# Kernel tuning notes

Hardware: AMD Instinct MI355X
Metric: run time of the kernel (lower is better)

## Reference

```python
import jax, jax.numpy as jnp
import numpy as np

NUM_ENTITIES = 100000
NUM_RELATIONS = 500
D = 256            # embedding_dim
T = 4              # num_hash_tables
H = 32             # hash_dim
B = 64             # batch of queries
K = 10
CAND = max(K * 10, int(NUM_ENTITIES * 0.1))  # = 10000


def setup_inputs() -> dict:
    key = jax.random.key(0)
    k0, k1, k2, k3, k4 = jax.random.split(key, 5)
    return {
        "head": jax.random.randint(k0, (B,), 0, NUM_ENTITIES),
        "relation": jax.random.randint(k1, (B,), 0, NUM_RELATIONS),
        "entity_emb": jax.random.normal(k2, (NUM_ENTITIES, D), jnp.float32) * 0.02,
        "relation_emb": jax.random.normal(k3, (NUM_RELATIONS, D), jnp.float32) * 0.02,
        "hash_proj": jax.random.normal(k4, (T, D, H), jnp.float32),
        "k": K,
    }


def reference(head, relation, entity_emb, relation_emb, hash_proj, k):
    # DistMult approximate query path of KnowledgeGraph.query (use_approximate=True).
    h = entity_emb[head]            # [B, D]
    r = relation_emb[relation]      # [B, D]
    target = h * r                  # DistMult target embedding [B, D]

    # LSH hash codes (0/1 floats): projected > 0
    thash = (jnp.einsum('bd,tdh->bth', target, hash_proj) > 0).astype(jnp.float32)      # [B,T,H]
    ahash = (jnp.einsum('nd,tdh->nth', entity_emb, hash_proj) > 0).astype(jnp.float32)  # [N,T,H]

    # Hamming distance over (T,H) bits without materializing [B,N,T,H]:
    # mismatches = sum(a) + sum(b) - 2 * <a,b>  for 0/1 codes
    dot = jnp.einsum('bth,nth->bn', thash, ahash)                                        # [B,N]
    hash_dist = thash.sum((1, 2))[:, None] + ahash.sum((1, 2))[None, :] - 2.0 * dot      # [B,N]

    # top num_candidates with SMALLEST hamming distance
    _, cand_idx = jax.lax.top_k(-hash_dist, CAND)                                        # [B,CAND]

    # DistMult score: (h*r*t).sum(-1) == target . t ; compute dense then gather candidates
    scores_all = jnp.einsum('bd,nd->bn', target, entity_emb)                             # [B,N]
    cand_scores = jnp.take_along_axis(scores_all, cand_idx, axis=1)                      # [B,CAND]

    top_scores, top_local = jax.lax.top_k(cand_scores, k)                                # [B,k]
    top_indices = jnp.take_along_axis(cand_idx, top_local, axis=1)                       # [B,k]
    return top_indices, top_scores
```

## Files before the change

kernel.cpp:

```cpp
#include <hip/hip_runtime.h>
#include <hip/hip_bf16.h>
#include <float.h>

constexpr int NENT  = 100000;
constexpr int DDIM  = 256;
constexpr int BQ    = 64;
constexpr int CANDN = 10000;
constexpr int KTOP  = 10;
constexpr int NSLICE = 16;
constexpr int SLICE  = 6272;
constexpr int HPAD   = 132;

typedef short v8s __attribute__((ext_vector_type(8)));
typedef float v4f __attribute__((ext_vector_type(4)));

__device__ inline void split3(float x, unsigned short& h0, unsigned short& h1,
                              unsigned short& h2) {
    unsigned t0 = __float_as_uint(x) & 0xffff0000u;
    float r1 = x - __uint_as_float(t0);
    unsigned t1 = __float_as_uint(r1) & 0xffff0000u;
    float r2 = r1 - __uint_as_float(t1);
    h0 = (unsigned short)(t0 >> 16);
    h1 = (unsigned short)(t1 >> 16);
    h2 = (unsigned short)(__float_as_uint(r2) >> 16);
}

__device__ inline void split8p(const float* p0, const float* p1,
                               v8s& o0, v8s& o1, v8s& o2) {
    union { v8s v; unsigned short u[8]; } r0, r1, r2;
    float4 f0 = *(const float4*)p0;
    float4 f1 = *(const float4*)(p1);
    float av[8] = {f0.x, f0.y, f0.z, f0.w, f1.x, f1.y, f1.z, f1.w};
    #pragma unroll
    for (int j = 0; j < 8; j++)
        split3(av[j], r0.u[j], r1.u[j], r2.u[j]);
    o0 = r0.v; o1 = r1.v; o2 = r2.v;
}

__device__ inline void stage16(const float* g, float* l) {
    __builtin_amdgcn_global_load_lds(
        (const __attribute__((address_space(1))) void*)g,
        (__attribute__((address_space(3))) void*)l, 16, 0, 0);
}

__global__ __launch_bounds__(256) void k_prep(
    const int* __restrict__ head, const int* __restrict__ rel,
    const float* __restrict__ E, const float* __restrict__ Rm,
    const float* __restrict__ proj,
    float* __restrict__ tgtT, unsigned* __restrict__ thash,
    unsigned short* __restrict__ Whi, unsigned short* __restrict__ Wmid,
    unsigned short* __restrict__ Wlo)
{
    __shared__ float tg[DDIM];
    int blk = blockIdx.x;
    int tid = threadIdx.x;
    if (blk < 128) {
        int c = blk, d = tid;
        float x = proj[((c >> 5)*DDIM + d)*32 + (c & 31)];
        unsigned short h0, h1, h2;
        split3(x, h0, h1, h2);
        Whi [c*DDIM + d] = h0;
        Wmid[c*DDIM + d] = h1;
        Wlo [c*DDIM + d] = h2;
    } else {
        int b = blk - 128;
        int h = head[b], r = rel[b];
        int d = tid;
        float v = E[h*DDIM + d] * Rm[r*DDIM + d];
        tg[d] = v;
        tgtT[d*BQ + b] = v;
        unsigned short h0, h1, h2;
        split3(v, h0, h1, h2);
        int c = 128 + b;
        Whi [c*DDIM + d] = h0;
        Wmid[c*DDIM + d] = h1;
        Wlo [c*DDIM + d] = h2;
        __syncthreads();
        if (tid < 128) {
            int t = tid >> 5, hh = tid & 31;
            float acc = 0.f;
            #pragma unroll 8
            for (int dd = 0; dd < DDIM; dd++)
                acc += tg[dd] * proj[(t*DDIM + dd)*32 + hh];
            unsigned long long m = __ballot(acc > 0.0f);
            int lane = tid & 63, w = tid >> 6;
            if (lane == 0) {
                thash[b*4 + w*2 + 0] = (unsigned)(m & 0xffffffffull);
                thash[b*4 + w*2 + 1] = (unsigned)(m >> 32);
            }
        }
    }
}

constexpr int TILE_E = 128;

__global__ __launch_bounds__(256, 2) void k_gemm(
    const float* __restrict__ E,
    const unsigned short* __restrict__ Whi, const unsigned short* __restrict__ Wmid,
    const unsigned short* __restrict__ Wlo,
    unsigned* __restrict__ ahash, float* __restrict__ scores)
{
    __shared__ __align__(16) float Af[2][TILE_E*32];
    unsigned short* bitsHalf = (unsigned short*)Af;

    int tid = threadIdx.x;
    int l = tid & 63, w = tid >> 6;
    int wm = w >> 1, wn = w & 1;
    int m = l & 15, quad = l >> 4;
    int n0 = blockIdx.x * TILE_E;

    const float* gsrc[4];
    #pragma unroll
    for (int it = 0; it < 4; it++) {
        int U = it*256 + tid;
        int row = U >> 3;
        int us  = (U & 7) ^ (row & 7);
        int n = n0 + row; if (n >= NENT) n = NENT - 1;
        gsrc[it] = E + (size_t)n*DDIM + us*4;
    }

    int offA0[4], offA1[4];
    #pragma unroll
    for (int a = 0; a < 4; a++) {
        int row = wm*64 + a*16 + m;
        offA0[a] = row*32 + (((2*quad)    ) ^ (m & 7))*4;
        offA1[a] = row*32 + (((2*quad) | 1) ^ (m & 7))*4;
    }

    int colOff[6];
    #pragma unroll
    for (int c = 0; c < 6; c++)
        colOff[c] = (wn*96 + c*16 + m)*DDIM + quad*8;

    v4f acc[4][6];
    #pragma unroll
    for (int a = 0; a < 4; a++)
        #pragma unroll
        for (int c = 0; c < 6; c++)
            acc[a][c] = (v4f)0.0f;

    #pragma unroll
    for (int it = 0; it < 4; it++)
        stage16(gsrc[it], &Af[0][(it*256 + w*64)*4]);
    __syncthreads();

    int bb = 0;
    for (int ch = 0; ch < DDIM/32; ch++) {
        if (ch + 1 < DDIM/32) {
            #pragma unroll
            for (int it = 0; it < 4; it++)
                stage16(gsrc[it] + (ch + 1)*32, &Af[bb ^ 1][(it*256 + w*64)*4]);
        }

        v8s a0[4], a1[4], a2[4];
        #pragma unroll
        for (int a = 0; a < 4; a++)
            split8p(&Af[bb][offA0[a]], &Af[bb][offA1[a]], a0[a], a1[a], a2[a]);

        int d0 = ch*32;
        #pragma unroll
        for (int c = 0; c < 6; c++) {
            int co = colOff[c] + d0;
            v8s b0 = *(const v8s*)(Whi  + co);
            v8s b1 = *(const v8s*)(Wmid + co);
            v8s b2 = *(const v8s*)(Wlo  + co);
            #pragma unroll
            for (int a = 0; a < 4; a++) {
                acc[a][c] = __builtin_amdgcn_mfma_f32_16x16x32_bf16(a2[a], b0, acc[a][c], 0, 0, 0);
                acc[a][c] = __builtin_amdgcn_mfma_f32_16x16x32_bf16(a0[a], b2, acc[a][c], 0, 0, 0);
                acc[a][c] = __builtin_amdgcn_mfma_f32_16x16x32_bf16(a1[a], b1, acc[a][c], 0, 0, 0);
                acc[a][c] = __builtin_amdgcn_mfma_f32_16x16x32_bf16(a1[a], b0, acc[a][c], 0, 0, 0);
                acc[a][c] = __builtin_amdgcn_mfma_f32_16x16x32_bf16(a0[a], b1, acc[a][c], 0, 0, 0);
                acc[a][c] = __builtin_amdgcn_mfma_f32_16x16x32_bf16(a0[a], b0, acc[a][c], 0, 0, 0);
            }
        }
        __syncthreads();
        bb ^= 1;
    }

    #pragma unroll
    for (int c = 0; c < 6; c++) {
        int ct = wn*6 + c;
        if (ct < 8) {
            #pragma unroll
            for (int a = 0; a < 4; a++) {
                #pragma unroll
                for (int r = 0; r < 4; r++) {
                    unsigned long long mb = __ballot(acc[a][c][r] > 0.0f);
                    if (m == 0) {
                        int rowl = wm*64 + a*16 + quad*4 + r;
                        bitsHalf[rowl*8 + ct] = (unsigned short)(mb >> (quad*16));
                    }
                }
            }
        } else {
            int b = ct*16 - 128 + m;
            #pragma unroll
            for (int a = 0; a < 4; a++) {
                int nb = n0 + wm*64 + a*16 + quad*4;
                if (nb < NENT)
                    *(float4*)(scores + (size_t)b*NENT + nb) = *(float4*)&acc[a][c];
            }
        }
    }
    __syncthreads();
    if (tid < TILE_E) {
        int n = n0 + tid;
        if (n < NENT)
            *(uint4*)(ahash + (size_t)n*4) = *(const uint4*)&bitsHalf[tid*8];
    }
}

__global__ __launch_bounds__(256) void k_dist(
    const unsigned* __restrict__ ahash, const unsigned* __restrict__ thash,
    unsigned char* __restrict__ dist8, unsigned short* __restrict__ histG)
{
    __shared__ unsigned hist[8][HPAD];
    int s = blockIdx.x, b = blockIdx.y, tid = threadIdx.x;
    int wv = tid >> 5;
    for (int i = tid; i < 8*HPAD; i += 256) ((unsigned*)hist)[i] = 0u;
    uint4 tw = *(const uint4*)(thash + b*4);
    __syncthreads();
    int n0 = s*SLICE;
    int n1 = n0 + SLICE; if (n1 > NENT) n1 = NENT;
    unsigned char* drow = dist8 + (size_t)b*NENT;
    for (int n = n0 + tid*4; n < n1; n += 1024) {
        int dv[4];
        #pragma unroll
        for (int i = 0; i < 4; i++) {
            uint4 a = *(const uint4*)(ahash + (size_t)(n+i)*4);
            dv[i] = __popc(a.x^tw.x) + __popc(a.y^tw.y) +
                    __popc(a.z^tw.z) + __popc(a.w^tw.w);
            atomicAdd(&hist[wv][dv[i]], 1u);
        }
        uchar4 o = make_uchar4((unsigned char)dv[0], (unsigned char)dv[1],
                               (unsigned char)dv[2], (unsigned char)dv[3]);
        *(uchar4*)(drow + n) = o;
    }
    __syncthreads();
    unsigned short* hrow = histG + ((size_t)b*NSLICE + s)*HPAD;
    for (int i = tid; i < 129; i += 256) {
        unsigned t = 0;
        #pragma unroll
        for (int v = 0; v < 8; v++) t += hist[v][i];
        hrow[i] = (unsigned short)t;
    }
}

__global__ __launch_bounds__(64) void k_cut(
    const unsigned char* __restrict__ dist8, const unsigned short* __restrict__ histG,
    int* __restrict__ dsG, int* __restrict__ ncG)
{
    __shared__ unsigned histT[HPAD];
    __shared__ int dsS, slS, rpS;
    int b = blockIdx.x, tid = threadIdx.x;
    for (int d = tid; d < 129; d += 64) {
        unsigned sum = 0;
        for (int s = 0; s < NSLICE; s++)
            sum += histG[((size_t)b*NSLICE + s)*HPAD + d];
        histT[d] = sum;
    }
    __syncthreads();
    if (tid == 0) {
        unsigned cum = 0; int ds = 128; unsigned R = 1;
        for (int d = 0; d < 129; d++) {
            unsigned c = cum + histT[d];
            if (c >= (unsigned)CANDN) { ds = d; R = (unsigned)CANDN - cum; break; }
            cum = c;
        }
        dsS = ds; dsG[b] = ds;
        unsigned acc = 0;
        for (int s = 0; s < NSLICE; s++) {
            unsigned c = histG[((size_t)b*NSLICE + s)*HPAD + ds];
            if (acc + c >= R) { slS = s; rpS = (int)(R - acc); break; }
            acc += c;
        }
    }
    __syncthreads();
    int ds = dsS;
    unsigned Rp = (unsigned)rpS;
    const unsigned char* drow = dist8 + (size_t)b*NENT;
    int sBase = slS*SLICE;
    int sEnd = sBase + SLICE; if (sEnd > NENT) sEnd = NENT;
    unsigned cnt = 0;
    for (int base = sBase; base < sEnd; base += 256) {
        unsigned char qa[4];
        #pragma unroll
        for (int s4 = 0; s4 < 4; s4++) {
            int n = base + s4*64 + tid;
            qa[s4] = (n < sEnd) ? drow[n] : (unsigned char)255;
        }
        bool done = false;
        #pragma unroll
        for (int s4 = 0; s4 < 4; s4++) {
            bool eq = (qa[s4] == (unsigned char)ds);
            unsigned long long mm = __ballot(eq);
            unsigned c = __popcll(mm);
            if (cnt + c >= Rp) {
                unsigned pre = __popcll(mm & ((1ull << tid) - 1ull));
                if (eq && (cnt + pre + 1u == Rp)) ncG[b] = base + s4*64 + tid;
                done = true; break;
            }
            cnt += c;
        }
        if (done) break;
    }
}

__global__ __launch_bounds__(256) void k_part(
    const unsigned char* __restrict__ dist8, const float* __restrict__ scores,
    const int* __restrict__ dsG, const int* __restrict__ ncG,
    const float* __restrict__ tgtT, const float* __restrict__ E,
    float* __restrict__ partS, int* __restrict__ partI)
{
    __shared__ float ls[256];
    __shared__ int   li[256];
    __shared__ float ps[112];
    __shared__ int   pi[112];
    __shared__ int   pcnt;
    __shared__ float TsS; __shared__ int TiS;
    __shared__ int   chosenI[KTOP];
    __shared__ float tgl[DDIM];

    int sl = blockIdx.x, b = blockIdx.y, tid = threadIdx.x;
    int ds = dsG[b], nc = ncG[b];
    const unsigned char* drow = dist8 + (size_t)b*NENT;
    const float* srow = scores + (size_t)b*NENT;
    int n0 = sl*SLICE;
    int n1 = n0 + SLICE; if (n1 > NENT) n1 = NENT;

    float topS[KTOP]; int topI[KTOP];
    #pragma unroll
    for (int i = 0; i < KTOP; i++) { topS[i] = -FLT_MAX; topI[i] = 0x7fffffff; }

    for (int n = n0 + tid*4; n < n1; n += 1024) {
        uchar4 dv = *(const uchar4*)(drow + n);
        unsigned char da[4] = {dv.x, dv.y, dv.z, dv.w};
        #pragma unroll
        for (int i = 0; i < 4; i++) {
            int d = da[i];
            int nn = n + i;
            if (d < ds || (d == ds && nn <= nc)) {
                float sc = srow[nn];
                if (sc > topS[KTOP-1]) {
                    int p = KTOP - 1;
                    while (p > 0 && topS[p-1] < sc) {
                        topS[p] = topS[p-1]; topI[p] = topI[p-1]; p--;
                    }
                    topS[p] = sc; topI[p] = nn;
                }
            }
        }
    }

    ls[tid] = topS[0]; li[tid] = topI[0];
    if (tid == 0) pcnt = 0;
    if (tid < 112) { ps[tid] = -FLT_MAX; pi[tid] = 0x7fffffff; }
    __syncthreads();

    float mv = topS[0]; int mi = topI[0];
    int rank = 0;
    for (int i = 0; i < 256; i++) {
        float v = ls[i]; int id = li[i];
        rank += (v > mv || (v == mv && id < mi)) ? 1 : 0;
    }
    if (rank == 9 || (rank < 9 && mi == 0x7fffffff)) { TsS = mv; TiS = mi; }
    __syncthreads();
    float ts = TsS; int ti = TiS;

    if (!(ts > mv || (ts == mv && ti < mi))) {
        #pragma unroll
        for (int j = 0; j < KTOP; j++) {
            float sj = topS[j]; int ij = topI[j];
            if (ij == 0x7fffffff) break;
            if (sj > ts || (sj == ts && ij <= ti)) {
                int p = atomicAdd(&pcnt, 1);
                ps[p] = sj; pi[p] = ij;
            } else break;
        }
    }
    __syncthreads();

    if (tid < 112) {
        float s = ps[tid]; int id = pi[tid];
        int r = 0;
        for (int i = 0; i < 112; i++) {
            float v = ps[i]; int iv = pi[i];
            bool beats = (v > s) || (v == s && (iv < id || (iv == id && i < tid)));
            r += beats ? 1 : 0;
        }
        if (r < KTOP) {
            chosenI[r] = id;
            partI[((size_t)b*NSLICE + sl)*KTOP + r] = id;
        }
    }

    for (int d = tid; d < DDIM; d += 256) tgl[d] = tgtT[d*BQ + b];
    __syncthreads();
    if (tid < KTOP) {
        int idx = chosenI[tid];
        float sc = -FLT_MAX;
        if (idx >= 0 && idx < NENT) {
            const float* er = E + (size_t)idx*DDIM;
            float acc = 0.f;
            #pragma unroll 8
            for (int d = 0; d < DDIM; d += 4) {
                float4 v = *(const float4*)(er + d);
                acc += v.x*tgl[d+0];
                acc += v.y*tgl[d+1];
                acc += v.z*tgl[d+2];
                acc += v.w*tgl[d+3];
            }
            sc = acc;
        }
        partS[((size_t)b*NSLICE + sl)*KTOP + tid] = sc;
    }
}

__global__ __launch_bounds__(256) void k_merge(
    const float* __restrict__ partS, const int* __restrict__ partI,
    float* __restrict__ out)
{
    __shared__ float sc2[NSLICE*KTOP];
    __shared__ int   ix2[NSLICE*KTOP];
    int b = blockIdx.x, tid = threadIdx.x;
    if (tid < NSLICE*KTOP) {
        sc2[tid] = partS[(size_t)b*NSLICE*KTOP + tid];
        ix2[tid] = partI[(size_t)b*NSLICE*KTOP + tid];
    }
    __syncthreads();
    if (tid < NSLICE*KTOP) {
        float mv = sc2[tid]; int mi = ix2[tid];
        int rank = 0;
        #pragma unroll 8
        for (int i = 0; i < NSLICE*KTOP; i++) {
            float v = sc2[i]; int id = ix2[i];
            bool beats = (v > mv) ||
                         (v == mv && (id < mi || (id == mi && i < tid)));
            rank += beats ? 1 : 0;
        }
        if (rank < KTOP) {
            out[b*KTOP + rank]           = (float)mi;
            out[BQ*KTOP + b*KTOP + rank] = mv;
        }
    }
}

extern "C" void kernel_launch(void* const* d_in, const int* in_sizes, int n_in,
                              void* d_out, int out_size, void* d_ws, size_t ws_size,
                              hipStream_t stream)
{
    const int*   head = (const int*)d_in[0];
    const int*   rel  = (const int*)d_in[1];
    const float* E    = (const float*)d_in[2];
    const float* Rm   = (const float*)d_in[3];
    const float* proj = (const float*)d_in[4];

    char* ws = (char*)d_ws;
    float*          tgtT   = (float*)(ws);
    unsigned*       thash  = (unsigned*)(ws + 65536);
    unsigned*       ahash  = (unsigned*)(ws + 66560);
    float*          scores = (float*)(ws + 1666560);
    unsigned char*  dist8  = (unsigned char*)(ws + 27266560);
    int*            dsG    = (int*)(ws + 33666560);
    int*            ncG    = (int*)(ws + 33666816);
    float*          partS  = (float*)(ws + 33667072);
    int*            partI  = (int*)(ws + 33708032);
    unsigned short* histG  = (unsigned short*)(ws + 33748992);
    unsigned short* Whi    = (unsigned short*)(ws + 34019328);
    unsigned short* Wmid   = (unsigned short*)(ws + 34117632);
    unsigned short* Wlo    = (unsigned short*)(ws + 34215936);
    float*          out    = (float*)d_out;

    hipLaunchKernelGGL(k_prep, dim3(192), dim3(256), 0, stream,
                       head, rel, E, Rm, proj, tgtT, thash, Whi, Wmid, Wlo);
    hipLaunchKernelGGL(k_gemm, dim3((NENT + TILE_E - 1)/TILE_E), dim3(256), 0, stream,
                       E, Whi, Wmid, Wlo, ahash, scores);
    hipLaunchKernelGGL(k_dist, dim3(NSLICE, BQ), dim3(256), 0, stream,
                       ahash, thash, dist8, histG);
    hipLaunchKernelGGL(k_cut, dim3(BQ), dim3(64), 0, stream,
                       dist8, histG, dsG, ncG);
    hipLaunchKernelGGL(k_part, dim3(NSLICE, BQ), dim3(256), 0, stream,
                       dist8, scores, dsG, ncG, tgtT, E, partS, partI);
    hipLaunchKernelGGL(k_merge, dim3(BQ), dim3(256), 0, stream,
                       partS, partI, out);
}
```

Baseline: 322.6 us.

## Fuse cutoff search into partition kernel and interleave histogram copies by lane

Removes the separate k_cut launch. Each k_part block now recomputes the distance threshold and the tie-break index from the slice histograms itself, which duplicates that work across the 16 slice blocks per query. The k_dist shared histogram is also re-laid out so that 8 copies are indexed by lane (tid&7) instead of by wavefront. This spreads atomic contention across copies and banks. The gain is one fewer kernel launch and less contention, paid for with a redundant serial scan in every partition block.

Result: no change. 318.4 us (-1.3%).

```diff
diff --git a/kernel.cpp b/kernel.cpp
--- a/kernel.cpp
+++ b/kernel.cpp
@@ -215,9 +215,9 @@
     const unsigned* __restrict__ ahash, const unsigned* __restrict__ thash,
     unsigned char* __restrict__ dist8, unsigned short* __restrict__ histG)
 {
-    __shared__ unsigned hist[8][HPAD];
+    __shared__ unsigned hist[HPAD][8];
     int s = blockIdx.x, b = blockIdx.y, tid = threadIdx.x;
-    int wv = tid >> 5;
+    int lv = tid & 7;
     for (int i = tid; i < 8*HPAD; i += 256) ((unsigned*)hist)[i] = 0u;
     uint4 tw = *(const uint4*)(thash + b*4);
     __syncthreads();
@@ -231,7 +231,7 @@
             uint4 a = *(const uint4*)(ahash + (size_t)(n+i)*4);
             dv[i] = __popc(a.x^tw.x) + __popc(a.y^tw.y) +
                     __popc(a.z^tw.z) + __popc(a.w^tw.w);
-            atomicAdd(&hist[wv][dv[i]], 1u);
+            atomicAdd(&hist[dv[i]][lv], 1u);
         }
         uchar4 o = make_uchar4((unsigned char)dv[0], (unsigned char)dv[1],
                                (unsigned char)dv[2], (unsigned char)dv[3]);
@@ -242,77 +242,19 @@
     for (int i = tid; i < 129; i += 256) {
         unsigned t = 0;
         #pragma unroll
-        for (int v = 0; v < 8; v++) t += hist[v][i];
+        for (int v = 0; v < 8; v++) t += hist[i][v];
         hrow[i] = (unsigned short)t;
-    }
-}
-
-__global__ __launch_bounds__(64) void k_cut(
-    const unsigned char* __restrict__ dist8, const unsigned short* __restrict__ histG,
-    int* __restrict__ dsG, int* __restrict__ ncG)
-{
-    __shared__ unsigned histT[HPAD];
-    __shared__ int dsS, slS, rpS;
-    int b = blockIdx.x, tid = threadIdx.x;
-    for (int d = tid; d < 129; d += 64) {
-        unsigned sum = 0;
-        for (int s = 0; s < NSLICE; s++)
-            sum += histG[((size_t)b*NSLICE + s)*HPAD + d];
-        histT[d] = sum;
-    }
-    __syncthreads();
-    if (tid == 0) {
-        unsigned cum = 0; int ds = 128; unsigned R = 1;
-        for (int d = 0; d < 129; d++) {
-            unsigned c = cum + histT[d];
-            if (c >= (unsigned)CANDN) { ds = d; R = (unsigned)CANDN - cum; break; }
-            cum = c;
-        }
-        dsS = ds; dsG[b] = ds;
-        unsigned acc = 0;
-        for (int s = 0; s < NSLICE; s++) {
-            unsigned c = histG[((size_t)b*NSLICE + s)*HPAD + ds];
-            if (acc + c >= R) { slS = s; rpS = (int)(R - acc); break; }
-            acc += c;
-        }
-    }
-    __syncthreads();
-    int ds = dsS;
-    unsigned Rp = (unsigned)rpS;
-    const unsigned char* drow = dist8 + (size_t)b*NENT;
-    int sBase = slS*SLICE;
-    int sEnd = sBase + SLICE; if (sEnd > NENT) sEnd = NENT;
-    unsigned cnt = 0;
-    for (int base = sBase; base < sEnd; base += 256) {
-        unsigned char qa[4];
-        #pragma unroll
-        for (int s4 = 0; s4 < 4; s4++) {
-            int n = base + s4*64 + tid;
-            qa[s4] = (n < sEnd) ? drow[n] : (unsigned char)255;
-        }
-        bool done = false;
-        #pragma unroll
-        for (int s4 = 0; s4 < 4; s4++) {
-            bool eq = (qa[s4] == (unsigned char)ds);
-            unsigned long long mm = __ballot(eq);
-            unsigned c = __popcll(mm);
-            if (cnt + c >= Rp) {
-                unsigned pre = __popcll(mm & ((1ull << tid) - 1ull));
-                if (eq && (cnt + pre + 1u == Rp)) ncG[b] = base + s4*64 + tid;
-                done = true; break;
-            }
-            cnt += c;
-        }
-        if (done) break;
     }
 }
 
 __global__ __launch_bounds__(256) void k_part(
     const unsigned char* __restrict__ dist8, const float* __restrict__ scores,
-    const int* __restrict__ dsG, const int* __restrict__ ncG,
+    const unsigned short* __restrict__ histG,
     const float* __restrict__ tgtT, const float* __restrict__ E,
     float* __restrict__ partS, int* __restrict__ partI)
 {
+    __shared__ unsigned histT[HPAD];
+    __shared__ int dsS, slS, rpS, ncS;
     __shared__ float ls[256];
     __shared__ int   li[256];
     __shared__ float ps[112];
@@ -323,9 +265,65 @@
     __shared__ float tgl[DDIM];
 
     int sl = blockIdx.x, b = blockIdx.y, tid = threadIdx.x;
-    int ds = dsG[b], nc = ncG[b];
     const unsigned char* drow = dist8 + (size_t)b*NENT;
     const float* srow = scores + (size_t)b*NENT;
+
+    for (int d = tid; d < 129; d += 256) {
+        unsigned sum = 0;
+        for (int s = 0; s < NSLICE; s++)
+            sum += histG[((size_t)b*NSLICE + s)*HPAD + d];
+        histT[d] = sum;
+    }
+    if (tid == 0) ncS = -1;
+    __syncthreads();
+    if (tid == 0) {
+        unsigned cum = 0; int dss = 128; unsigned R = 1;
+        for (int d = 0; d < 129; d++) {
+            unsigned c = cum + histT[d];
+            if (c >= (unsigned)CANDN) { dss = d; R = (unsigned)CANDN - cum; break; }
+            cum = c;
+        }
+        dsS = dss;
+        unsigned acc = 0; slS = NSLICE - 1; rpS = 1;
+        for (int s = 0; s < NSLICE; s++) {
+            unsigned c = histG[((size_t)b*NSLICE + s)*HPAD + dss];
+            if (acc + c >= R) { slS = s; rpS = (int)(R - acc); break; }
+            acc += c;
+        }
+    }
+    __syncthreads();
+    if (tid < 64) {
+        int dss = dsS;
+        unsigned Rp = (unsigned)rpS;
+        int sBase = slS*SLICE;
+        int sEnd = sBase + SLICE; if (sEnd > NENT) sEnd = NENT;
+        unsigned cnt = 0;
+        for (int base = sBase; base < sEnd; base += 256) {
+            unsigned char qa[4];
+            #pragma unroll
+            for (int s4 = 0; s4 < 4; s4++) {
+                int n = base + s4*64 + tid;
+                qa[s4] = (n < sEnd) ? drow[n] : (unsigned char)255;
+            }
+            bool done = false;
+            #pragma unroll
+            for (int s4 = 0; s4 < 4; s4++) {
+                bool eq = (qa[s4] == (unsigned char)dss);
+                unsigned long long mm = __ballot(eq);
+                unsigned c = __popcll(mm);
+                if (cnt + c >= Rp) {
+                    unsigned pre = __popcll(mm & ((1ull << tid) - 1ull));
+                    if (eq && (cnt + pre + 1u == Rp)) ncS = base + s4*64 + tid;
+                    done = true; break;
+                }
+                cnt += c;
+            }
+            if (done) break;
+        }
+    }
+    __syncthreads();
+    int ds = dsS, nc = ncS;
+
     int n0 = sl*SLICE;
     int n1 = n0 + SLICE; if (n1 > NENT) n1 = NENT;
 
@@ -462,8 +460,6 @@
     unsigned*       ahash  = (unsigned*)(ws + 66560);
     float*          scores = (float*)(ws + 1666560);
     unsigned char*  dist8  = (unsigned char*)(ws + 27266560);
-    int*            dsG    = (int*)(ws + 33666560);
-    int*            ncG    = (int*)(ws + 33666816);
     float*          partS  = (float*)(ws + 33667072);
     int*            partI  = (int*)(ws + 33708032);
     unsigned short* histG  = (unsigned short*)(ws + 33748992);
@@ -478,10 +474,8 @@
                        E, Whi, Wmid, Wlo, ahash, scores);
     hipLaunchKernelGGL(k_dist, dim3(NSLICE, BQ), dim3(256), 0, stream,
                        ahash, thash, dist8, histG);
-    hipLaunchKernelGGL(k_cut, dim3(BQ), dim3(64), 0, stream,
-                       dist8, histG, dsG, ncG);
     hipLaunchKernelGGL(k_part, dim3(NSLICE, BQ), dim3(256), 0, stream,
-                       dist8, scores, dsG, ncG, tgtT, E, partS, partI);
+                       dist8, scores, histG, tgtT, E, partS, partI);
     hipLaunchKernelGGL(k_merge, dim3(BQ), dim3(256), 0, stream,
                        partS, partI, out);
 }
```
